# Kernel tuning notes

Measured on AMD Instinct MI355X. Metric: run time of the kernel, lower is better.

Reference implementation:

```python
import jax, jax.numpy as jnp
import numpy as np

N = 8  # fixed node count per sample (hardcoded in the torch module)


def setup_inputs() -> dict:
    key = jax.random.key(0)
    ks = jax.random.split(key, 13)
    B = 131072

    def w(k, shape, fan_in):
        # torch nn.Linear default init: U(-1/sqrt(fan_in), 1/sqrt(fan_in))
        return jax.random.uniform(k, shape, jnp.float32, -1.0, 1.0) / np.sqrt(fan_in).astype(np.float32)

    return {
        "x": jax.random.normal(ks[0], (B, N), jnp.float32),
        "enc_w1": w(ks[1], (3, 64), 3),   "enc_b1": w(ks[2], (64,), 3),
        "enc_w2": w(ks[3], (64, 2), 64),  "enc_b2": w(ks[4], (2,), 64),
        "gcn1_w": w(ks[5], (2, 32), 2),   "gcn1_b": w(ks[6], (32,), 2),
        "gcn2_w": w(ks[7], (32, 32), 32), "gcn2_b": w(ks[8], (32,), 32),
        "dec_w1": w(ks[9], (32, 64), 32), "dec_b1": w(ks[10], (64,), 32),
        "dec_w2": w(ks[11], (64, 3), 64), "dec_b2": w(ks[12], (3,), 64),
    }


def _gabriel_norm_adj(p):
    """Batched Gabriel graph -> GCN-normalized (A + I) with unit edge weights.

    p: (B, N, 2) latent 2D points.
    Edge (i,j) exists iff no other point k lies strictly inside the circle
    with diameter (p_i, p_j)  (dist(p_k, mid)^2 < r^2, matching torch's '<').
    Gabriel graphs contain the nearest-neighbor graph, so for N>=2 edges always
    exist and the torch fallback branch is unreachable.
    Returns D^{-1/2} (A + I) D^{-1/2} of shape (B, N, N) (GCNConv default:
    add_self_loops=True with weight 1, symmetric normalization).
    """
    mid = (p[:, :, None, :] + p[:, None, :, :]) * 0.5                 # (B,N,N,2)
    r2 = jnp.sum((p[:, :, None, :] - mid) ** 2, axis=-1)              # (B,N,N)
    # d2[b,i,j,k] = ||p[b,k] - mid[b,i,j]||^2  -> (B,N,N,N), the big intermediate
    d2 = jnp.sum((p[:, None, None, :, :] - mid[:, :, :, None, :]) ** 2, axis=-1)
    a = jnp.arange(N)
    k_not_ij = (a[None, None, :] != a[:, None, None]) & (a[None, None, :] != a[None, :, None])  # (N,N,N) [i,j,k]
    blocked = jnp.any((d2 < r2[..., None]) & k_not_ij, axis=-1)       # (B,N,N)
    off_diag = a[:, None] != a[None, :]
    adj = ((~blocked) & off_diag).astype(p.dtype)                     # symmetric Gabriel adjacency
    a_hat = adj + jnp.eye(N, dtype=p.dtype)                           # self-loops, weight 1
    dinv = jax.lax.rsqrt(jnp.sum(a_hat, axis=-1))                     # (B,N)
    return dinv[:, :, None] * a_hat * dinv[:, None, :]


def reference(x, enc_w1, enc_b1, enc_w2, enc_b2,
              gcn1_w, gcn1_b, gcn2_w, gcn2_b,
              dec_w1, dec_b1, dec_w2, dec_b2):
    B = x.shape[0]
    idx = jnp.arange(N, dtype=x.dtype)
    # preprocess: (B, N, 3) rows [0, value, index]
    xp = jnp.stack([jnp.zeros_like(x), x, jnp.broadcast_to(idx, x.shape)], axis=-1)
    latent = jax.nn.relu(xp @ enc_w1 + enc_b1) @ enc_w2 + enc_b2      # (B,N,2)
    # torch builds the graph from detach().cpu().numpy() -> no grad through structure
    norm = jax.lax.stop_gradient(_gabriel_norm_adj(latent))           # (B,N,N)
    h1 = jax.nn.relu(jnp.einsum('bij,bjf->bif', norm, latent @ gcn1_w) + gcn1_b)  # (B,N,32)
    h2 = jnp.einsum('bij,bjf->bif', norm, h1 @ gcn2_w) + gcn2_b                    # (B,N,32)
    pooled = jnp.mean(h2, axis=1)                                     # (B,32)
    node = jnp.broadcast_to(pooled[:, None, :], (B, N, pooled.shape[-1]))
    dec = jax.nn.relu(node @ dec_w1 + dec_b1) @ dec_w2 + dec_b2       # (B,N,3)
    reconstructed = dec[:, :, 1]                                      # (B,N)
    return reconstructed, latent
```

## Files before the change

kernel.cpp:

```cpp
#include <hip/hip_runtime.h>


typedef float v2 __attribute__((ext_vector_type(2)));
static __device__ __forceinline__ v2 sp(float s) { return (v2){s, s}; }
static __device__ __forceinline__ v2 fma2(v2 a, v2 b, v2 c) {
    return __builtin_elementwise_fma(a, b, c);
}
static __device__ __forceinline__ v2 ldv2(const float* p) {
    return *reinterpret_cast<const v2*>(p);
}

__global__ __launch_bounds__(256) void gae_aux(
    const float* __restrict__ gcn2_w, const float* __restrict__ gcn2_b,
    const float* __restrict__ dec_w1, const float* __restrict__ dec_b1,
    const float* __restrict__ dec_w2, const float* __restrict__ enc_w1,
    const float* __restrict__ enc_b1, float* __restrict__ ws)
{
    const int tid = blockIdx.x * 256 + threadIdx.x;
    const int f = tid >> 6, h = tid & 63;
    float acc = 0.0f;
    #pragma unroll 8
    for (int g = 0; g < 32; ++g)
        acc = fmaf(gcn2_w[f * 32 + g], dec_w1[g * 64 + h], acc);
    ws[f * 64 + h] = acc;
    if (tid < 64) {
        float c = dec_b1[h];
        #pragma unroll 8
        for (int g = 0; g < 32; ++g)
            c = fmaf(gcn2_b[g], dec_w1[g * 64 + h], c);
        ws[2048 + h] = c;
        ws[2112 + h] = dec_w2[h * 3 + 1];
    }
    if (tid < 512) {
        const int hh = tid >> 3, ii = tid & 7;
        ws[2176 + tid] = fmaf((float)ii, enc_w1[128 + hh], enc_b1[hh]);
    }
}

template <int I, int J>
static __device__ __forceinline__ void gpair(const v2* __restrict__ p,
                                             unsigned& ml, unsigned& mh)
{
    #pragma clang fp contract(off)
    v2 mid = (p[I] + p[J]) * sp(0.5f);
    v2 di = p[I] - mid;  v2 si = di * di;  float r2i = si.x + si.y;
    v2 dj = p[J] - mid;  v2 sj = dj * dj;  float r2j = sj.x + sj.y;
    float dmin = 3.4e38f;
    #pragma unroll
    for (int k = 0; k < 8; ++k) {
        if (k == I || k == J) continue;
        v2 dk = p[k] - mid;
        v2 sk = dk * dk;
        dmin = fminf(dmin, sk.x + sk.y);
    }
    constexpr unsigned bi = 1u << (((I & 3) * 8) + J);
    constexpr unsigned bj = 1u << (((J & 3) * 8) + I);
    if (I < 4) ml |= (dmin < r2i) ? 0u : bi; else mh |= (dmin < r2i) ? 0u : bi;
    if (J < 4) ml |= (dmin < r2j) ? 0u : bj; else mh |= (dmin < r2j) ? 0u : bj;
}

__global__ __launch_bounds__(256, 8) void gae_main(
    const float* __restrict__ x,
    const float* __restrict__ enc_w1,
    const float* __restrict__ enc_w2,
    const float* __restrict__ enc_b2,
    const float* __restrict__ gcn1_w,
    const float* __restrict__ gcn1_b,
    const float* __restrict__ ws,
    const float* __restrict__ dec_b2,
    float* __restrict__ out_rec,
    float* __restrict__ out_lat,
    int B)
{
    __shared__ union { v2 p[8][64]; v2 t[16][64]; } ptb;
    __shared__ union { unsigned m[4][2][64]; float o[4][64]; } mob;
    __shared__ v2    nbuf[8][64];
    __shared__ float cjbuf[8][64];

    const int lane = threadIdx.x & 63;
    const int ru   = __builtin_amdgcn_readfirstlane(threadIdx.x >> 6);
    int g = blockIdx.x * 64 + lane;
    if (g >= B) g = B - 1;

    const float2 xr = *reinterpret_cast<const float2*>(x + (size_t)g * 8 + 2 * ru);
    const v2 xp2 = (v2){xr.x, xr.y};

    const float* ctab = ws + 2176;
    v2 pl0, pl1;
    { const v2 b2v = ldv2(enc_b2); pl0 = b2v; pl1 = b2v; }
    #pragma unroll 8
    for (int h = 0; h < 64; ++h) {
        const float wx = enc_w1[64 + h];
        const v2 uxy = ldv2(enc_w2 + 2 * h);
        const v2 cpr = ldv2(ctab + h * 8 + 2 * ru);
        v2 t = fma2(xp2, sp(wx), cpr);
        float t0 = fmaxf(t.x, 0.0f);
        float t1 = fmaxf(t.y, 0.0f);
        pl0 = fma2(sp(t0), uxy, pl0);
        pl1 = fma2(sp(t1), uxy, pl1);
    }

    ptb.p[2 * ru + 0][lane] = pl0;
    ptb.p[2 * ru + 1][lane] = pl1;
    __syncthreads();
    v2 p[8];
    #pragma unroll
    for (int j = 0; j < 8; ++j) p[j] = ptb.p[j][lane];

    unsigned ml = 0u, mh = 0u;
    if (ru == 0) {
        gpair<0,1>(p, ml, mh); gpair<0,2>(p, ml, mh); gpair<0,3>(p, ml, mh);
        gpair<0,4>(p, ml, mh); gpair<0,5>(p, ml, mh); gpair<0,6>(p, ml, mh);
        gpair<0,7>(p, ml, mh);
    } else if (ru == 1) {
        gpair<1,2>(p, ml, mh); gpair<1,3>(p, ml, mh); gpair<1,4>(p, ml, mh);
        gpair<1,5>(p, ml, mh); gpair<1,6>(p, ml, mh); gpair<1,7>(p, ml, mh);
        gpair<2,3>(p, ml, mh);
    } else if (ru == 2) {
        gpair<2,4>(p, ml, mh); gpair<2,5>(p, ml, mh); gpair<2,6>(p, ml, mh);
        gpair<2,7>(p, ml, mh); gpair<3,4>(p, ml, mh); gpair<3,5>(p, ml, mh);
        gpair<3,6>(p, ml, mh);
    } else {
        gpair<3,7>(p, ml, mh); gpair<4,5>(p, ml, mh); gpair<4,6>(p, ml, mh);
        gpair<4,7>(p, ml, mh); gpair<5,6>(p, ml, mh); gpair<5,7>(p, ml, mh);
        gpair<6,7>(p, ml, mh);
    }

    mob.m[ru][0][lane] = ml;
    mob.m[ru][1][lane] = mh;
    __syncthreads();
    ml = (mob.m[0][0][lane] | mob.m[1][0][lane]) |
         (mob.m[2][0][lane] | mob.m[3][0][lane]) | 0x08040201u;
    mh = (mob.m[0][1][lane] | mob.m[1][1][lane]) |
         (mob.m[2][1][lane] | mob.m[3][1][lane]) | 0x80402010u;

    float dinv[8];
    v2 q[8];
    #pragma unroll
    for (int i = 0; i < 8; ++i) {
        const unsigned rb = ((i < 4 ? ml : mh) >> ((i & 3) * 8)) & 0xffu;
        dinv[i] = __builtin_amdgcn_rsqf((float)__popc(rb));
        q[i] = sp(dinv[i]) * p[i];
    }

    {
        const unsigned w = (ru < 2) ? ml : mh;
        const int sh = ((2 * ru) & 3) * 8;
        const unsigned rb0 = (w >> sh) & 0xffu;
        const unsigned rb1 = (w >> (sh + 8)) & 0xffu;
        const float dv0 = __builtin_amdgcn_rsqf((float)__popc(rb0));
        const float dv1 = __builtin_amdgcn_rsqf((float)__popc(rb1));
        v2 a0 = sp(0.0f), a1 = sp(0.0f);
        #pragma unroll
        for (int j = 0; j < 8; ++j) {
            a0 = fma2(sp((float)((rb0 >> j) & 1u)), q[j], a0);
            a1 = fma2(sp((float)((rb1 >> j) & 1u)), q[j], a1);
        }
        nbuf[2 * ru + 0][lane] = sp(dv0) * a0;
        nbuf[2 * ru + 1][lane] = sp(dv1) * a1;

        const int j0 = 2 * ru, j1 = 2 * ru + 1;
        float s0 = 0.0f, s1 = 0.0f;
        #pragma unroll
        for (int i = 0; i < 8; ++i) {
            const unsigned rb = ((i < 4 ? ml : mh) >> ((i & 3) * 8)) & 0xffu;
            s0 = fmaf((float)((rb >> j0) & 1u), dinv[i], s0);
            s1 = fmaf((float)((rb >> j1) & 1u), dinv[i], s1);
        }
        cjbuf[j0][lane] = 0.125f * dv0 * s0;
        cjbuf[j1][lane] = 0.125f * dv1 * s1;
    }
    __syncthreads();

    const float* w0 = gcn1_w + 8 * ru;
    const float* w1 = gcn1_w + 32 + 8 * ru;
    const float* bl = gcn1_b + 8 * ru;
    v2 t2[4];
    #pragma unroll
    for (int fp = 0; fp < 4; ++fp) t2[fp] = sp(0.0f);
    #pragma unroll
    for (int i = 0; i < 8; ++i) {
        const v2 ni = nbuf[i][lane];
        const float ci = cjbuf[i][lane];
        const v2 nxi = sp(ni.x), nyi = sp(ni.y), civ = sp(ci);
        #pragma unroll
        for (int fp = 0; fp < 4; ++fp) {
            v2 h = fma2(nxi, ldv2(w0 + 2 * fp),
                   fma2(nyi, ldv2(w1 + 2 * fp), ldv2(bl + 2 * fp)));
            h = __builtin_elementwise_max(h, sp(0.0f));
            t2[fp] = fma2(civ, h, t2[fp]);
        }
    }

    #pragma unroll
    for (int fp = 0; fp < 4; ++fp) ptb.t[4 * ru + fp][lane] = t2[fp];
    __syncthreads();

    const float* Wd = ws + 16 * ru;
    const float* cd = ws + 2048 + 16 * ru;
    const float* w2 = ws + 2112 + 16 * ru;
    v2 a2[8];
    #pragma unroll
    for (int hp = 0; hp < 8; ++hp) a2[hp] = ldv2(cd + 2 * hp);
    __builtin_amdgcn_s_setprio(1);
    #pragma unroll
    for (int fp = 0; fp < 16; ++fp) {
        const v2 tv = ptb.t[fp][lane];
        const float* wrA = Wd + (2 * fp) * 64;
        const float* wrB = Wd + (2 * fp + 1) * 64;
        const v2 tA = sp(tv.x), tB = sp(tv.y);
        #pragma unroll
        for (int hp = 0; hp < 8; ++hp) {
            a2[hp] = fma2(tA, ldv2(wrA + 2 * hp), a2[hp]);
            a2[hp] = fma2(tB, ldv2(wrB + 2 * hp), a2[hp]);
        }
    }
    __builtin_amdgcn_s_setprio(0);
    v2 oacc = sp(0.0f);
    #pragma unroll
    for (int hp = 0; hp < 8; ++hp) {
        v2 rr = __builtin_elementwise_max(a2[hp], sp(0.0f));
        oacc = fma2(rr, ldv2(w2 + 2 * hp), oacc);
    }
    const float opart = oacc.x + oacc.y;

    mob.o[ru][lane] = opart;
    __syncthreads();
    const float outv = ((mob.o[0][lane] + mob.o[1][lane]) +
                        (mob.o[2][lane] + mob.o[3][lane])) + dec_b2[1];

    *reinterpret_cast<float4*>(out_lat + (size_t)g * 16 + 4 * ru) =
        make_float4(pl0.x, pl0.y, pl1.x, pl1.y);
    *reinterpret_cast<float2*>(out_rec + (size_t)g * 8 + 2 * ru) =
        make_float2(outv, outv);
}

extern "C" void kernel_launch(void* const* d_in, const int* in_sizes, int n_in,
                              void* d_out, int out_size, void* d_ws, size_t ws_size,
                              hipStream_t stream) {
    const float* x       = (const float*)d_in[0];
    const float* enc_w1  = (const float*)d_in[1];
    const float* enc_b1  = (const float*)d_in[2];
    const float* enc_w2  = (const float*)d_in[3];
    const float* enc_b2  = (const float*)d_in[4];
    const float* gcn1_w  = (const float*)d_in[5];
    const float* gcn1_b  = (const float*)d_in[6];
    const float* gcn2_w  = (const float*)d_in[7];
    const float* gcn2_b  = (const float*)d_in[8];
    const float* dec_w1  = (const float*)d_in[9];
    const float* dec_b1  = (const float*)d_in[10];
    const float* dec_w2  = (const float*)d_in[11];
    const float* dec_b2  = (const float*)d_in[12];

    const int B = in_sizes[0] / 8;
    float* out_rec = (float*)d_out;
    float* out_lat = out_rec + (size_t)B * 8;
    float* ws      = (float*)d_ws;

    gae_aux<<<8, 256, 0, stream>>>(gcn2_w, gcn2_b, dec_w1, dec_b1, dec_w2,
                                   enc_w1, enc_b1, ws);

    const int blocks = (B + 63) / 64;
    gae_main<<<blocks, 256, 0, stream>>>(
        x, enc_w1, enc_w2, enc_b2,
        gcn1_w, gcn1_b, ws, dec_b2,
        out_rec, out_lat, B);
}
```

Measured before the change: 106.7 us.

## Drop auxiliary weight-folding kernel and compute gcn2 and decoder per sample

Removes the separate launch that folded gcn2_w into dec_w1 and precomputed encoder bias tables. The main kernel now applies gcn2 explicitly, adding a 32x32 matmul stage, then the decoder with the raw weights, and folds the bias table into the encoder loop. Shared memory is rebuilt as one aliased buffer. The aim is to save a kernel launch and its dependency, at the cost of roughly double the per-sample FMA work in the tail plus an extra barrier.

```diff
diff --git a/kernel.cpp b/kernel.cpp
--- a/kernel.cpp
+++ b/kernel.cpp
@@ -8,33 +8,6 @@
 }
 static __device__ __forceinline__ v2 ldv2(const float* p) {
     return *reinterpret_cast<const v2*>(p);
-}
-
-__global__ __launch_bounds__(256) void gae_aux(
-    const float* __restrict__ gcn2_w, const float* __restrict__ gcn2_b,
-    const float* __restrict__ dec_w1, const float* __restrict__ dec_b1,
-    const float* __restrict__ dec_w2, const float* __restrict__ enc_w1,
-    const float* __restrict__ enc_b1, float* __restrict__ ws)
-{
-    const int tid = blockIdx.x * 256 + threadIdx.x;
-    const int f = tid >> 6, h = tid & 63;
-    float acc = 0.0f;
-    #pragma unroll 8
-    for (int g = 0; g < 32; ++g)
-        acc = fmaf(gcn2_w[f * 32 + g], dec_w1[g * 64 + h], acc);
-    ws[f * 64 + h] = acc;
-    if (tid < 64) {
-        float c = dec_b1[h];
-        #pragma unroll 8
-        for (int g = 0; g < 32; ++g)
-            c = fmaf(gcn2_b[g], dec_w1[g * 64 + h], c);
-        ws[2048 + h] = c;
-        ws[2112 + h] = dec_w2[h * 3 + 1];
-    }
-    if (tid < 512) {
-        const int hh = tid >> 3, ii = tid & 7;
-        ws[2176 + tid] = fmaf((float)ii, enc_w1[128 + hh], enc_b1[hh]);
-    }
 }
 
 template <int I, int J>
@@ -62,20 +35,28 @@
 __global__ __launch_bounds__(256, 8) void gae_main(
     const float* __restrict__ x,
     const float* __restrict__ enc_w1,
+    const float* __restrict__ enc_b1,
     const float* __restrict__ enc_w2,
     const float* __restrict__ enc_b2,
     const float* __restrict__ gcn1_w,
     const float* __restrict__ gcn1_b,
-    const float* __restrict__ ws,
+    const float* __restrict__ gcn2_w,
+    const float* __restrict__ gcn2_b,
+    const float* __restrict__ dec_w1,
+    const float* __restrict__ dec_b1,
+    const float* __restrict__ dec_w2,
     const float* __restrict__ dec_b2,
     float* __restrict__ out_rec,
     float* __restrict__ out_lat,
     int B)
 {
-    __shared__ union { v2 p[8][64]; v2 t[16][64]; } ptb;
-    __shared__ union { unsigned m[4][2][64]; float o[4][64]; } mob;
-    __shared__ v2    nbuf[8][64];
-    __shared__ float cjbuf[8][64];
+    __shared__ __align__(16) float smem[4096];
+    v2*       const A2 = reinterpret_cast<v2*>(smem);
+    unsigned* const MB = reinterpret_cast<unsigned*>(smem + 2048);
+    v2*       const N2 = reinterpret_cast<v2*>(smem + 2560);
+    float*    const CJ = smem + 3584;
+    float*    const PL = smem + 2048;
+    float*    const OO = smem;
 
     const int lane = threadIdx.x & 63;
     const int ru   = __builtin_amdgcn_readfirstlane(threadIdx.x >> 6);
@@ -84,28 +65,31 @@
 
     const float2 xr = *reinterpret_cast<const float2*>(x + (size_t)g * 8 + 2 * ru);
     const v2 xp2 = (v2){xr.x, xr.y};
-
-    const float* ctab = ws + 2176;
+    const float i0f = (float)(2 * ru), i1f = i0f + 1.0f;
+
     v2 pl0, pl1;
     { const v2 b2v = ldv2(enc_b2); pl0 = b2v; pl1 = b2v; }
     #pragma unroll 8
     for (int h = 0; h < 64; ++h) {
         const float wx = enc_w1[64 + h];
+        const float wi = enc_w1[128 + h];
+        const float bb = enc_b1[h];
         const v2 uxy = ldv2(enc_w2 + 2 * h);
-        const v2 cpr = ldv2(ctab + h * 8 + 2 * ru);
-        v2 t = fma2(xp2, sp(wx), cpr);
+        const float c0 = fmaf(i0f, wi, bb);
+        const float c1 = fmaf(i1f, wi, bb);
+        v2 t = fma2(xp2, sp(wx), (v2){c0, c1});
         float t0 = fmaxf(t.x, 0.0f);
         float t1 = fmaxf(t.y, 0.0f);
         pl0 = fma2(sp(t0), uxy, pl0);
         pl1 = fma2(sp(t1), uxy, pl1);
     }
 
-    ptb.p[2 * ru + 0][lane] = pl0;
-    ptb.p[2 * ru + 1][lane] = pl1;
+    A2[(2 * ru + 0) * 64 + lane] = pl0;
+    A2[(2 * ru + 1) * 64 + lane] = pl1;
     __syncthreads();
     v2 p[8];
     #pragma unroll
-    for (int j = 0; j < 8; ++j) p[j] = ptb.p[j][lane];
+    for (int j = 0; j < 8; ++j) p[j] = A2[j * 64 + lane];
 
     unsigned ml = 0u, mh = 0u;
     if (ru == 0) {
@@ -126,13 +110,13 @@
         gpair<6,7>(p, ml, mh);
     }
 
-    mob.m[ru][0][lane] = ml;
-    mob.m[ru][1][lane] = mh;
-    __syncthreads();
-    ml = (mob.m[0][0][lane] | mob.m[1][0][lane]) |
-         (mob.m[2][0][lane] | mob.m[3][0][lane]) | 0x08040201u;
-    mh = (mob.m[0][1][lane] | mob.m[1][1][lane]) |
-         (mob.m[2][1][lane] | mob.m[3][1][lane]) | 0x80402010u;
+    MB[ru * 128 +  0 + lane] = ml;
+    MB[ru * 128 + 64 + lane] = mh;
+    __syncthreads();
+    ml = (MB[0 * 128 + lane] | MB[1 * 128 + lane]) |
+         (MB[2 * 128 + lane] | MB[3 * 128 + lane]) | 0x08040201u;
+    mh = (MB[0 * 128 + 64 + lane] | MB[1 * 128 + 64 + lane]) |
+         (MB[2 * 128 + 64 + lane] | MB[3 * 128 + 64 + lane]) | 0x80402010u;
 
     float dinv[8];
     v2 q[8];
@@ -156,8 +140,8 @@
             a0 = fma2(sp((float)((rb0 >> j) & 1u)), q[j], a0);
             a1 = fma2(sp((float)((rb1 >> j) & 1u)), q[j], a1);
         }
-        nbuf[2 * ru + 0][lane] = sp(dv0) * a0;
-        nbuf[2 * ru + 1][lane] = sp(dv1) * a1;
+        N2[(2 * ru + 0) * 64 + lane] = sp(dv0) * a0;
+        N2[(2 * ru + 1) * 64 + lane] = sp(dv1) * a1;
 
         const int j0 = 2 * ru, j1 = 2 * ru + 1;
         float s0 = 0.0f, s1 = 0.0f;
@@ -167,8 +151,8 @@
             s0 = fmaf((float)((rb >> j0) & 1u), dinv[i], s0);
             s1 = fmaf((float)((rb >> j1) & 1u), dinv[i], s1);
         }
-        cjbuf[j0][lane] = 0.125f * dv0 * s0;
-        cjbuf[j1][lane] = 0.125f * dv1 * s1;
+        CJ[j0 * 64 + lane] = 0.125f * dv0 * s0;
+        CJ[j1 * 64 + lane] = 0.125f * dv1 * s1;
     }
     __syncthreads();
 
@@ -180,8 +164,8 @@
     for (int fp = 0; fp < 4; ++fp) t2[fp] = sp(0.0f);
     #pragma unroll
     for (int i = 0; i < 8; ++i) {
-        const v2 ni = nbuf[i][lane];
-        const float ci = cjbuf[i][lane];
+        const v2 ni = N2[i * 64 + lane];
+        const float ci = CJ[i * 64 + lane];
         const v2 nxi = sp(ni.x), nyi = sp(ni.y), civ = sp(ci);
         #pragma unroll
         for (int fp = 0; fp < 4; ++fp) {
@@ -193,41 +177,61 @@
     }
 
     #pragma unroll
-    for (int fp = 0; fp < 4; ++fp) ptb.t[4 * ru + fp][lane] = t2[fp];
-    __syncthreads();
-
-    const float* Wd = ws + 16 * ru;
-    const float* cd = ws + 2048 + 16 * ru;
-    const float* w2 = ws + 2112 + 16 * ru;
+    for (int fp = 0; fp < 4; ++fp) A2[(4 * ru + fp) * 64 + lane] = t2[fp];
+    __syncthreads();
+
+    v2 pg2[4];
+    #pragma unroll
+    for (int kp = 0; kp < 4; ++kp) pg2[kp] = ldv2(gcn2_b + 8 * ru + 2 * kp);
+    #pragma unroll
+    for (int fp = 0; fp < 16; ++fp) {
+        const v2 tv = A2[fp * 64 + lane];
+        #pragma unroll
+        for (int half = 0; half < 2; ++half) {
+            const int f = 2 * fp + half;
+            const v2 tf = sp(half ? tv.y : tv.x);
+            const float* wr = gcn2_w + f * 32 + 8 * ru;
+            #pragma unroll
+            for (int kp = 0; kp < 4; ++kp)
+                pg2[kp] = fma2(tf, ldv2(wr + 2 * kp), pg2[kp]);
+        }
+    }
+    #pragma unroll
+    for (int kp = 0; kp < 4; ++kp) {
+        PL[(8 * ru + 2 * kp + 0) * 64 + lane] = pg2[kp].x;
+        PL[(8 * ru + 2 * kp + 1) * 64 + lane] = pg2[kp].y;
+    }
+    __syncthreads();
+
+    const float* db = dec_b1 + 16 * ru;
     v2 a2[8];
     #pragma unroll
-    for (int hp = 0; hp < 8; ++hp) a2[hp] = ldv2(cd + 2 * hp);
+    for (int hp = 0; hp < 8; ++hp) a2[hp] = ldv2(db + 2 * hp);
     __builtin_amdgcn_s_setprio(1);
     #pragma unroll
-    for (int fp = 0; fp < 16; ++fp) {
-        const v2 tv = ptb.t[fp][lane];
-        const float* wrA = Wd + (2 * fp) * 64;
-        const float* wrB = Wd + (2 * fp + 1) * 64;
-        const v2 tA = sp(tv.x), tB = sp(tv.y);
-        #pragma unroll
-        for (int hp = 0; hp < 8; ++hp) {
-            a2[hp] = fma2(tA, ldv2(wrA + 2 * hp), a2[hp]);
-            a2[hp] = fma2(tB, ldv2(wrB + 2 * hp), a2[hp]);
-        }
+    for (int f = 0; f < 32; ++f) {
+        const float pf = PL[f * 64 + lane];
+        const v2 pfv = sp(pf);
+        const float* wr = dec_w1 + f * 64 + 16 * ru;
+        #pragma unroll
+        for (int hp = 0; hp < 8; ++hp)
+            a2[hp] = fma2(pfv, ldv2(wr + 2 * hp), a2[hp]);
     }
     __builtin_amdgcn_s_setprio(0);
     v2 oacc = sp(0.0f);
     #pragma unroll
     for (int hp = 0; hp < 8; ++hp) {
         v2 rr = __builtin_elementwise_max(a2[hp], sp(0.0f));
-        oacc = fma2(rr, ldv2(w2 + 2 * hp), oacc);
+        const int h0 = 16 * ru + 2 * hp;
+        const v2 wv = (v2){dec_w2[h0 * 3 + 1], dec_w2[h0 * 3 + 4]};
+        oacc = fma2(rr, wv, oacc);
     }
     const float opart = oacc.x + oacc.y;
 
-    mob.o[ru][lane] = opart;
-    __syncthreads();
-    const float outv = ((mob.o[0][lane] + mob.o[1][lane]) +
-                        (mob.o[2][lane] + mob.o[3][lane])) + dec_b2[1];
+    OO[ru * 64 + lane] = opart;
+    __syncthreads();
+    const float outv = ((OO[lane] + OO[64 + lane]) +
+                        (OO[128 + lane] + OO[192 + lane])) + dec_b2[1];
 
     *reinterpret_cast<float4*>(out_lat + (size_t)g * 16 + 4 * ru) =
         make_float4(pl0.x, pl0.y, pl1.x, pl1.y);
@@ -255,14 +259,12 @@
     const int B = in_sizes[0] / 8;
     float* out_rec = (float*)d_out;
     float* out_lat = out_rec + (size_t)B * 8;
-    float* ws      = (float*)d_ws;
-
-    gae_aux<<<8, 256, 0, stream>>>(gcn2_w, gcn2_b, dec_w1, dec_b1, dec_w2,
-                                   enc_w1, enc_b1, ws);
+    (void)d_ws; (void)ws_size;
 
     const int blocks = (B + 63) / 64;
     gae_main<<<blocks, 256, 0, stream>>>(
-        x, enc_w1, enc_w2, enc_b2,
-        gcn1_w, gcn1_b, ws, dec_b2,
+        x, enc_w1, enc_b1, enc_w2, enc_b2,
+        gcn1_w, gcn1_b, gcn2_w, gcn2_b,
+        dec_w1, dec_b1, dec_w2, dec_b2,
         out_rec, out_lat, B);
 }
```

New measurement: 106.1 us. Within noise of the previous version (-0.6%).
